# Kernel optimization log

Measured on AMD Instinct MI355X. Metric: run time of the kernel, lower is better.

## Reference

```python
import jax, jax.numpy as jnp
import numpy as np

N = 50000      # nodes
E = 400000     # edges
G = 128        # graphs in batch
D_NODE = 64
EDGE_DIM = 72
HEADS = 4
H0, H1, H2 = 128, 128, 64
NC = 2
NEG = 0.2      # GATConv leaky_relu negative_slope default
D1 = H2 + EDGE_DIM - 1  # ffn input dim = 135


def _p(k, shape, s=0.1):
    return jax.random.normal(k, shape, dtype=jnp.float32) * s


def setup_inputs() -> dict:
    key = jax.random.key(0)
    ks = jax.random.split(key, 24)
    x = jax.random.normal(ks[0], (N, D_NODE), dtype=jnp.float32)
    edge_index = jax.random.randint(ks[1], (2, E), 0, N)
    edge_attr = jax.random.uniform(ks[2], (E, EDGE_DIM), dtype=jnp.float32)
    batch = jnp.sort(jax.random.randint(ks[3], (N,), 0, G))
    return dict(
        x=x, edge_index=edge_index, edge_attr=edge_attr, batch=batch,
        # GATConv layer 1: in=D_NODE, out=H0, heads=HEADS, concat
        W1=_p(ks[4], (D_NODE, HEADS * H0)), We1=_p(ks[5], (EDGE_DIM, HEADS * H0)),
        as1=_p(ks[6], (HEADS, H0)), ad1=_p(ks[7], (HEADS, H0)), ae1=_p(ks[8], (HEADS, H0)),
        b1=jnp.zeros((HEADS * H0,), jnp.float32),
        # GATConv layer 2: in=HEADS*H0, out=H1, heads=HEADS, concat
        W2=_p(ks[9], (HEADS * H0, HEADS * H1)), We2=_p(ks[10], (EDGE_DIM, HEADS * H1)),
        as2=_p(ks[11], (HEADS, H1)), ad2=_p(ks[12], (HEADS, H1)), ae2=_p(ks[13], (HEADS, H1)),
        b2=jnp.zeros((HEADS * H1,), jnp.float32),
        # GATConv layer 3: in=HEADS*H1, out=H2, heads=1, concat=False
        W3=_p(ks[14], (HEADS * H1, H2)), We3=_p(ks[15], (EDGE_DIM, H2)),
        as3=_p(ks[16], (1, H2)), ad3=_p(ks[17], (1, H2)), ae3=_p(ks[18], (1, H2)),
        b3=jnp.zeros((H2,), jnp.float32),
        # ffn: Linear(135 -> 67), ReLU, Linear(67 -> 2), Softmax
        Wf1=_p(ks[19], (D1, D1 // 2)), bf1=jnp.zeros((D1 // 2,), jnp.float32),
        Wf2=_p(ks[20], (D1 // 2, NC)), bf2=jnp.zeros((NC,), jnp.float32),
    )


def _seg_softmax(s, seg, n):
    # numerically-stable softmax over segments (per-destination neighborhoods)
    m = jax.ops.segment_max(s, seg, num_segments=n)
    m = jnp.where(jnp.isfinite(m), m, 0.0)
    e = jnp.exp(s - m[seg])
    z = jax.ops.segment_sum(e, seg, num_segments=n)
    return e / (z[seg] + 1e-16)


def _gat(x, src, dst, eattr, W, We, a_s, a_d, a_e, b, heads, oc, concat):
    # PyG GATConv with edge_dim: shared src/dst projection, edge feats only in attention
    n = x.shape[0]
    xs = (x @ W).reshape(n, heads, oc)            # [N,H,C]
    ee = (eattr @ We).reshape(-1, heads, oc)      # [Ea,H,C]
    alpha = (xs * a_s).sum(-1)[src] + (xs * a_d).sum(-1)[dst] + (ee * a_e).sum(-1)
    alpha = jax.nn.leaky_relu(alpha, NEG)         # [Ea,H]
    alpha = _seg_softmax(alpha, dst, n)
    out = jax.ops.segment_sum(xs[src] * alpha[:, :, None], dst, num_segments=n)
    out = out.reshape(n, heads * oc) if concat else out.mean(axis=1)
    return out + b


def reference(x, edge_index, edge_attr, batch,
              W1, We1, as1, ad1, ae1, b1,
              W2, We2, as2, ad2, ae2, b2,
              W3, We3, as3, ad3, ae3, b3,
              Wf1, bf1, Wf2, bf2):
    src, dst = edge_index[0], edge_index[1]
    n = x.shape[0]
    # --- 1-gram feature vector: scatter-add edge_attr[:, :-1] by graph of src ---
    eb = batch[src]
    og = jax.ops.segment_sum(edge_attr[:, :-1], eb, num_segments=G)   # [G, EDGE_DIM-1]
    og = og / jnp.maximum(jnp.linalg.norm(og, axis=1, keepdims=True), 1e-12)
    # --- add self loops, edge_attr fill_value='mean' (mean over incoming edges) ---
    ones_e = jnp.ones((src.shape[0],), x.dtype)
    deg = jax.ops.segment_sum(ones_e, dst, num_segments=n)
    loop_attr = jax.ops.segment_sum(edge_attr, dst, num_segments=n) / jnp.maximum(deg, 1.0)[:, None]
    nodes = jnp.arange(n)
    src_a = jnp.concatenate([src, nodes])
    dst_a = jnp.concatenate([dst, nodes])
    ea = jnp.concatenate([edge_attr, loop_attr], axis=0)
    # --- GAT stack with ReLU activations ---
    h = jax.nn.relu(_gat(x, src_a, dst_a, ea, W1, We1, as1, ad1, ae1, b1, HEADS, H0, True))
    h = jax.nn.relu(_gat(h, src_a, dst_a, ea, W2, We2, as2, ad2, ae2, b2, HEADS, H1, True))
    h = jax.nn.relu(_gat(h, src_a, dst_a, ea, W3, We3, as3, ad3, ae3, b3, 1, H2, False))
    # --- global mean pool over graphs ---
    cnt = jax.ops.segment_sum(jnp.ones((n,), x.dtype), batch, num_segments=G)
    pooled = jax.ops.segment_sum(h, batch, num_segments=G) / jnp.maximum(cnt, 1.0)[:, None]
    # --- concat + ffn (dropout p=0 in eval) + softmax ---
    z = jnp.concatenate([pooled, og], axis=1)                         # [G, 135]
    z = jax.nn.relu(z @ Wf1 + bf1)
    return jax.nn.softmax(z @ Wf2 + bf2, axis=1)
```

## Files before the change

kernel.cpp:

```cpp
#include <hip/hip_runtime.h>

#define NNODES 50000
#define NEDGES 400000
#define NEA    450000
#define NG     128
#define DEGCAP 96
#define OGW    72

typedef unsigned short u16;
typedef unsigned int   u32;
typedef __attribute__((ext_vector_type(8))) short short8v;
typedef __attribute__((ext_vector_type(4))) float f32x4;

static inline int ceil_div(int a, int b){ return (a + b - 1)/b; }

__device__ __forceinline__ u16 f2bf(float f){
  u32 u = __builtin_bit_cast(u32, f);
  u = (u + 0x7fffu + ((u >> 16) & 1u)) >> 16;
  return (u16)u;
}
__device__ __forceinline__ float bfLO(u32 q){ return __builtin_bit_cast(float, q << 16); }
__device__ __forceinline__ float bfHI(u32 q){ return __builtin_bit_cast(float, q & 0xffff0000u); }
__device__ __forceinline__ void gload_lds16(const u16* g, u16* l){
  __builtin_amdgcn_global_load_lds((const __attribute__((address_space(1))) void*)g,
                                   (__attribute__((address_space(3))) void*)l, 16, 0, 0);
}

__global__ void k_prep(const float* __restrict__ x, u16* __restrict__ xb,
                       const float* __restrict__ W1, u16* __restrict__ Wt1,
                       const float* __restrict__ W2, u16* __restrict__ Wt2,
                       const float* __restrict__ W3, u16* __restrict__ Wt3,
                       const float* __restrict__ We1, const float* __restrict__ ae1,
                       const float* __restrict__ We2, const float* __restrict__ ae2,
                       const float* __restrict__ We3, const float* __restrict__ ae3,
                       float* __restrict__ veall){
  int i = blockIdx.x*blockDim.x + threadIdx.x;
  if (i < 800000){
    float4 v = ((const float4*)x)[i];
    ((ushort4*)xb)[i] = make_ushort4(f2bf(v.x), f2bf(v.y), f2bf(v.z), f2bf(v.w));
    return;
  }
  i -= 800000;
  if (i < 32768){
    int n = i >> 6, k = i & 63;
    Wt1[i] = f2bf(W1[(size_t)k*512 + n]);
    return;
  }
  i -= 32768;
  if (i < 262144){
    int n = i >> 9, k = i & 511;
    Wt2[i] = f2bf(W2[(size_t)k*512 + n]);
    return;
  }
  i -= 262144;
  if (i < 32768){
    int n = i >> 9, k = i & 511;
    Wt3[i] = f2bf(W3[(size_t)k*64 + n]);
    return;
  }
  i -= 32768;
  if (i < 648){
    const float* We; const float* ae; int H, C, basej, li;
    if (i < 288){ We = We1; ae = ae1; H = 4; C = 128; basej = 0; li = i; }
    else if (i < 576){ We = We2; ae = ae2; H = 4; C = 128; basej = 4; li = i - 288; }
    else { We = We3; ae = ae3; H = 1; C = 64; basej = 8; li = i - 576; }
    int k = li / H, h = li - k*H;
    const float* wrow = We + (size_t)k*H*C + (size_t)h*C;
    const float* arow = ae + (size_t)h*C;
    float s = 0.f;
    for (int c = 0; c < C; ++c) s += wrow[c]*arow[c];
    veall[k*9 + basej + h] = s;
  }
}

__global__ void k_deg_gb(const int* __restrict__ src, const int* __restrict__ dst,
                         const int* __restrict__ batch,
                         int* __restrict__ deg, int* __restrict__ gb, int* __restrict__ gcnt){
  __shared__ int h[NG];
  int t = threadIdx.x;
  if (t < NG) h[t] = 0;
  __syncthreads();
  int e = blockIdx.x*blockDim.x + t;
  if (e < NEDGES){
    atomicAdd(&deg[dst[e]], 1);
    int g = batch[src[e]];
    gb[e] = g;
    atomicAdd(&h[g], 1);
  }
  __syncthreads();
  if (t < NG && h[t]) atomicAdd(&gcnt[t], h[t]);
}

__global__ __launch_bounds__(1024) void k_scans(const int* __restrict__ deg, int* __restrict__ off,
                                                const int* __restrict__ gcnt, int* __restrict__ goff,
                                                int* __restrict__ gcur){
  __shared__ int s[1024];
  int t = threadIdx.x;
  if (blockIdx.x == 0){
    const int CH = (NNODES + 1023)/1024;
    int i0 = t*CH, i1 = min(i0 + CH, NNODES);
    int loc = 0;
    for (int i = i0; i < i1; ++i) loc += deg[i] + 1;
    s[t] = loc; __syncthreads();
    for (int o = 1; o < 1024; o <<= 1){
      int v = (t >= o) ? s[t-o] : 0;
      __syncthreads();
      s[t] += v;
      __syncthreads();
    }
    int excl = s[t] - loc;
    for (int i = i0; i < i1; ++i){ off[i] = excl; excl += deg[i] + 1; }
    if (t == 1023) off[NNODES] = s[1023];
  } else {
    int v = 0;
    if (t < NG){ v = gcnt[t]; s[t] = v; }
    __syncthreads();
    for (int o = 1; o < NG; o <<= 1){
      int x = 0;
      if (t < NG && t >= o) x = s[t-o];
      __syncthreads();
      if (t < NG) s[t] += x;
      __syncthreads();
    }
    if (t < NG){ goff[t] = s[t] - v; gcur[t] = s[t] - v; }
  }
}

__global__ void k_scatter(const int* __restrict__ src, const int* __restrict__ dst,
                          const int* __restrict__ gb, const int* __restrict__ off,
                          int* __restrict__ cnt, int* __restrict__ gcur,
                          int* __restrict__ csr_src, int* __restrict__ edgepos,
                          int* __restrict__ sortedeid){
  __shared__ int lcnt[NG];
  __shared__ int lbase[NG];
  int t = threadIdx.x;
  int e = blockIdx.x*256 + t;
  if (t < NG) lcnt[t] = 0;
  __syncthreads();
  int g = -1, lr = 0;
  if (e < NEDGES){
    int d = dst[e];
    int p = off[d] + atomicAdd(&cnt[d], 1);
    csr_src[p] = src[e];
    edgepos[e] = p;
    g = gb[e];
    lr = atomicAdd(&lcnt[g], 1);
  } else {
    int n2 = e - NEDGES;
    if (n2 < NNODES){
      int p = off[n2+1] - 1;
      csr_src[p] = n2;
    }
  }
  __syncthreads();
  if (t < NG && lcnt[t]) lbase[t] = atomicAdd(&gcur[t], lcnt[t]);
  __syncthreads();
  if (g >= 0) sortedeid[lbase[g] + lr] = e;
}

__global__ __launch_bounds__(256) void k_og2(const float* __restrict__ attr,
    const int* __restrict__ goff, const int* __restrict__ gcnt,
    const int* __restrict__ sortedeid, float* __restrict__ og){
  __shared__ float red[16][OGW];
  int g = blockIdx.x >> 4, chunk = blockIdx.x & 15;
  int lane = threadIdx.x & 63, w = threadIdx.x >> 6;
  int esub = lane >> 4, l16 = lane & 15;
  int slot = w*4 + esub;
  int beg = goff[g], cnt = gcnt[g];
  int cbeg = beg + ((cnt*chunk) >> 4);
  int cend = beg + ((cnt*(chunk+1)) >> 4);
  f32x4 acc  = {0.f,0.f,0.f,0.f};
  f32x4 acch = {0.f,0.f,0.f,0.f};
  for (int i0 = cbeg; i0 < cend; i0 += 32){
    int e1 = i0 + slot, e2 = i0 + 16 + slot;
    int id1 = (e1 < cend) ? sortedeid[e1] : -1;
    int id2 = (e2 < cend) ? sortedeid[e2] : -1;
    f32x4 v1 = {0.f,0.f,0.f,0.f}, v2 = {0.f,0.f,0.f,0.f};
    f32x4 h1 = {0.f,0.f,0.f,0.f}, h2 = {0.f,0.f,0.f,0.f};
    if (id1 >= 0){
      v1 = *(const f32x4*)(attr + (size_t)id1*72 + l16*4);
      if (l16 < 2) h1 = *(const f32x4*)(attr + (size_t)id1*72 + 64 + l16*4);
    }
    if (id2 >= 0){
      v2 = *(const f32x4*)(attr + (size_t)id2*72 + l16*4);
      if (l16 < 2) h2 = *(const f32x4*)(attr + (size_t)id2*72 + 64 + l16*4);
    }
    acc += v1; acc += v2;
    if (l16 < 2){ acch += h1; acch += h2; }
  }
  #pragma unroll
  for (int j = 0; j < 4; ++j) red[slot][l16*4 + j] = acc[j];
  if (l16 < 2){
    #pragma unroll
    for (int j = 0; j < 4; ++j) red[slot][64 + l16*4 + j] = acch[j];
  }
  __syncthreads();
  int t = threadIdx.x;
  if (t < 71){
    float s = 0.f;
    #pragma unroll
    for (int q = 0; q < 16; ++q) s += red[q][t];
    atomicAdd(&og[g*OGW + t], s);
  }
}

__global__ __launch_bounds__(256) void k_se_all(const float* __restrict__ attr,
    const int* __restrict__ edgepos, const float* __restrict__ veall,
    float* __restrict__ se1, float* __restrict__ se2, float* __restrict__ se3){
  __shared__ float vel[72*9];
  for (int i = threadIdx.x; i < 72*9; i += blockDim.x) vel[i] = veall[i];
  __syncthreads();
  int e = blockIdx.x*blockDim.x + threadIdx.x;
  if (e >= NEDGES) return;
  const float4* row = (const float4*)(attr + (size_t)e*72);
  float s[9];
  #pragma unroll
  for (int j = 0; j < 9; ++j) s[j] = 0.f;
  #pragma unroll
  for (int kk = 0; kk < 18; ++kk){
    float4 a = row[kk];
    #pragma unroll
    for (int j = 0; j < 9; ++j)
      s[j] += a.x*vel[(kk*4+0)*9+j] + a.y*vel[(kk*4+1)*9+j]
            + a.z*vel[(kk*4+2)*9+j] + a.w*vel[(kk*4+3)*9+j];
  }
  int p = edgepos[e];
  *(float4*)(se1 + (size_t)p*4) = make_float4(s[0], s[1], s[2], s[3]);
  *(float4*)(se2 + (size_t)p*4) = make_float4(s[4], s[5], s[6], s[7]);
  se3[p] = s[8];
}

__global__ __launch_bounds__(256) void k_gemm128(const u16* __restrict__ A,
    const u16* __restrict__ Bt, u16* __restrict__ C, int M, int K,
    const float* __restrict__ a_s, const float* __restrict__ a_d,
    float* __restrict__ ssrc, float* __restrict__ sdst){
  __shared__ __align__(16) u16 smem[128*128];
  u16* As = smem;
  u16* Bs = smem + 128*64;
  __shared__ float s_ps[128][2];
  __shared__ float s_pd[128][2];
  const int tid = threadIdx.x;
  const int wid = tid >> 6, lane = tid & 63;
  const int l15 = lane & 15, kslot = lane >> 4;
  const int wr = wid >> 1, wc = wid & 1;
  const int h = blockIdx.x;
  const int m0 = blockIdx.y * 128, n0 = h * 128;
  const int Nn = 512;
  f32x4 acc[4][4];
  #pragma unroll
  for (int mi = 0; mi < 4; ++mi)
    #pragma unroll
    for (int ni = 0; ni < 4; ++ni)
      acc[mi][ni] = (f32x4){0.f,0.f,0.f,0.f};

  for (int kt = 0; kt < K; kt += 64){
    #pragma unroll
    for (int r = 0; r < 4; ++r){
      int chunk = (r*4 + wid)*64 + lane;
      int row = chunk >> 3, c8 = chunk & 7;
      int srcc = c8 ^ (row & 7);
      int grow = m0 + row; if (grow > M-1) grow = M-1;
      gload_lds16(A + (size_t)grow*K + kt + srcc*8, &As[chunk*8]);
    }
    #pragma unroll
    for (int r = 0; r < 4; ++r){
      int chunk = (r*4 + wid)*64 + lane;
      int row = chunk >> 3, c8 = chunk & 7;
      int srcc = c8 ^ (row & 7);
      gload_lds16(Bt + (size_t)(n0+row)*K + kt + srcc*8, &Bs[chunk*8]);
    }
    __syncthreads();
    #pragma unroll
    for (int s = 0; s < 2; ++s){
      short8v a[4], b[4];
      #pragma unroll
      for (int mi = 0; mi < 4; ++mi){
        int row = wr*64 + mi*16 + l15;
        a[mi] = *(const short8v*)(&As[row*64 + (((s*4 + kslot) ^ (row&7))*8)]);
      }
      #pragma unroll
      for (int ni = 0; ni < 4; ++ni){
        int col = wc*64 + ni*16 + l15;
        b[ni] = *(const short8v*)(&Bs[col*64 + (((s*4 + kslot) ^ (col&7))*8)]);
      }
      #pragma unroll
      for (int mi = 0; mi < 4; ++mi)
        #pragma unroll
        for (int ni = 0; ni < 4; ++ni)
          acc[mi][ni] = __builtin_amdgcn_mfma_f32_16x16x32_bf16(a[mi], b[ni], acc[mi][ni], 0, 0, 0);
    }
    __syncthreads();
  }
  float asv[4], adv[4];
  #pragma unroll
  for (int ni = 0; ni < 4; ++ni){
    int c = wc*64 + ni*16 + l15;
    asv[ni] = a_s[h*128 + c];
    adv[ni] = a_d[h*128 + c];
  }
  #pragma unroll
  for (int mi = 0; mi < 4; ++mi){
    #pragma unroll
    for (int r = 0; r < 4; ++r){
      int row_l = wr*64 + mi*16 + kslot*4 + r;
      float ps = 0.f, pd = 0.f;
      #pragma unroll
      for (int ni = 0; ni < 4; ++ni){
        float v = acc[mi][ni][r];
        smem[row_l*128 + wc*64 + ni*16 + l15] = f2bf(v);
        ps += v*asv[ni];
        pd += v*adv[ni];
      }
      #pragma unroll
      for (int m = 8; m >= 1; m >>= 1){ ps += __shfl_xor(ps,m); pd += __shfl_xor(pd,m); }
      if (l15 == 0){ s_ps[row_l][wc] = ps; s_pd[row_l][wc] = pd; }
    }
  }
  __syncthreads();
  #pragma unroll
  for (int i = 0; i < 8; ++i){
    int c = i*256 + tid;
    int row = c >> 4, c16 = c & 15;
    int grow = m0 + row;
    if (grow < M)
      *(uint4*)(C + (size_t)grow*Nn + n0 + c16*8) = *(const uint4*)(&smem[row*128 + c16*8]);
  }
  if (tid < 128){
    int grow = m0 + tid;
    if (grow < M){
      ssrc[grow*4 + h] = s_ps[tid][0] + s_ps[tid][1];
      sdst[grow*4 + h] = s_pd[tid][0] + s_pd[tid][1];
    }
  }
}

__global__ __launch_bounds__(256) void k_gemm64(const u16* __restrict__ A,
    const u16* __restrict__ Bt, u16* __restrict__ C, int M,
    const float* __restrict__ a_s, const float* __restrict__ a_d,
    float* __restrict__ ssrc, float* __restrict__ sdst){
  __shared__ __align__(16) u16 As[64*64];
  __shared__ __align__(16) u16 Bs[64*64];
  const int tid = threadIdx.x;
  const int wid = tid >> 6, lane = tid & 63;
  const int l15 = lane & 15, kslot = lane >> 4;
  const int m0 = blockIdx.x * 64;
  f32x4 acc[4];
  #pragma unroll
  for (int ni = 0; ni < 4; ++ni) acc[ni] = (f32x4){0.f,0.f,0.f,0.f};
  for (int kt = 0; kt < 512; kt += 64){
    #pragma unroll
    for (int r = 0; r < 2; ++r){
      int chunk = r*256 + tid;
      int row = chunk >> 3, c8 = chunk & 7;
      int srcc = c8 ^ (row & 7);
      int grow = m0 + row; if (grow > M-1) grow = M-1;
      gload_lds16(A + (size_t)grow*512 + kt + srcc*8, &As[chunk*8]);
    }
    #pragma unroll
    for (int r = 0; r < 2; ++r){
      int chunk = r*256 + tid;
      int row = chunk >> 3, c8 = chunk & 7;
      int srcc = c8 ^ (row & 7);
      gload_lds16(Bt + (size_t)row*512 + kt + srcc*8, &Bs[chunk*8]);
    }
    __syncthreads();
    #pragma unroll
    for (int s = 0; s < 2; ++s){
      int row = wid*16 + l15;
      short8v a = *(const short8v*)(&As[row*64 + (((s*4 + kslot) ^ (row&7))*8)]);
      #pragma unroll
      for (int ni = 0; ni < 4; ++ni){
        int col = ni*16 + l15;
        short8v b = *(const short8v*)(&Bs[col*64 + (((s*4 + kslot) ^ (col&7))*8)]);
        acc[ni] = __builtin_amdgcn_mfma_f32_16x16x32_bf16(a, b, acc[ni], 0, 0, 0);
      }
    }
    __syncthreads();
  }
  #pragma unroll
  for (int r = 0; r < 4; ++r){
    int row_l = wid*16 + kslot*4 + r;
    int grow = m0 + row_l;
    float ps = 0.f, pd = 0.f;
    #pragma unroll
    for (int ni = 0; ni < 4; ++ni){
      float v = acc[ni][r];
      int c = ni*16 + l15;
      As[row_l*64 + c] = f2bf(v);
      ps += v*a_s[c];
      pd += v*a_d[c];
    }
    #pragma unroll
    for (int m = 8; m >= 1; m >>= 1){ ps += __shfl_xor(ps,m); pd += __shfl_xor(pd,m); }
    if (l15 == 0 && grow < M){ ssrc[grow] = ps; sdst[grow] = pd; }
  }
  __syncthreads();
  #pragma unroll
  for (int i = 0; i < 2; ++i){
    int c = i*256 + tid;
    int row = c >> 3, c8 = c & 7;
    int grow = m0 + row;
    if (grow < M)
      *(uint4*)(C + (size_t)grow*64 + c8*8) = *(const uint4*)(&As[row*64 + c8*8]);
  }
}

__global__ __launch_bounds__(256) void k_agg12(const u16* __restrict__ xs,
    const int* __restrict__ off, const int* __restrict__ csr_src,
    const float* __restrict__ ssrc, const float* __restrict__ sdst,
    const float* __restrict__ sep,
    const float* __restrict__ bias, u16* __restrict__ out){
  __shared__ float s_al[4][DEGCAP][4];
  __shared__ int   s_col[4][DEGCAP];
  int w = threadIdx.x >> 6, lane = threadIdx.x & 63;
  int n = blockIdx.x*4 + w;
  int beg = off[n];
  int deg = off[n+1] - beg;
  if (deg > DEGCAP) deg = DEGCAP;
  int es = lane >> 2, h = lane & 3;
  float sd = sdst[n*4+h];
  float sesum = 0.f;
  for (int e0 = 0; e0 < deg-1; e0 += 16){
    int e = e0 + es;
    if (e < deg-1){
      int col = csr_src[beg+e];
      float sr = sep[(size_t)(beg+e)*4 + h];
      sesum += sr;
      float s = ssrc[col*4+h] + sd + sr;
      s = (s > 0.f) ? s : 0.2f*s;
      s_al[w][e][h] = s;
      if (h == 0) s_col[w][e] = col;
    }
  }
  #pragma unroll
  for (int msk = 4; msk < 64; msk <<= 1) sesum += __shfl_xor(sesum, msk);
  if (es == 0){
    float slp = sesum / fmaxf((float)(deg-1), 1.0f);
    float s = ssrc[n*4+h] + sd + slp;
    s = (s > 0.f) ? s : 0.2f*s;
    s_al[w][deg-1][h] = s;
    if (h == 0) s_col[w][deg-1] = n;
  }
  float m = -1e30f;
  for (int e = es; e < deg; e += 16) m = fmaxf(m, s_al[w][e][h]);
  #pragma unroll
  for (int msk = 4; msk < 64; msk <<= 1) m = fmaxf(m, __shfl_xor(m, msk));
  float z = 0.f;
  for (int e = es; e < deg; e += 16){ float ex = __expf(s_al[w][e][h]-m); s_al[w][e][h] = ex; z += ex; }
  #pragma unroll
  for (int msk = 4; msk < 64; msk <<= 1) z += __shfl_xor(z, msk);
  float inv = 1.0f/(z + 1e-16f);
  for (int e = es; e < deg; e += 16) s_al[w][e][h] *= inv;
  int degR = (deg + 3) & ~3;
  for (int e = deg + es; e < degR; e += 16){ s_al[w][e][h] = 0.f; if (h == 0) s_col[w][e] = n; }
  __syncthreads();
  int hh = lane >> 4;
  f32x4 accA = {0.f,0.f,0.f,0.f}, accB = {0.f,0.f,0.f,0.f};
  for (int e = 0; e < degR; e += 4){
    int c0 = s_col[w][e+0], c1 = s_col[w][e+1], c2 = s_col[w][e+2], c3 = s_col[w][e+3];
    uint4 q0 = *(const uint4*)(xs + (size_t)c0*512 + lane*8);
    uint4 q1 = *(const uint4*)(xs + (size_t)c1*512 + lane*8);
    uint4 q2 = *(const uint4*)(xs + (size_t)c2*512 + lane*8);
    uint4 q3 = *(const uint4*)(xs + (size_t)c3*512 + lane*8);
    float a0 = s_al[w][e+0][hh], a1 = s_al[w][e+1][hh];
    float a2 = s_al[w][e+2][hh], a3 = s_al[w][e+3][hh];
    accA[0] += a0*bfLO(q0.x) + a1*bfLO(q1.x) + a2*bfLO(q2.x) + a3*bfLO(q3.x);
    accA[1] += a0*bfHI(q0.x) + a1*bfHI(q1.x) + a2*bfHI(q2.x) + a3*bfHI(q3.x);
    accA[2] += a0*bfLO(q0.y) + a1*bfLO(q1.y) + a2*bfLO(q2.y) + a3*bfLO(q3.y);
    accA[3] += a0*bfHI(q0.y) + a1*bfHI(q1.y) + a2*bfHI(q2.y) + a3*bfHI(q3.y);
    accB[0] += a0*bfLO(q0.z) + a1*bfLO(q1.z) + a2*bfLO(q2.z) + a3*bfLO(q3.z);
    accB[1] += a0*bfHI(q0.z) + a1*bfHI(q1.z) + a2*bfHI(q2.z) + a3*bfHI(q3.z);
    accB[2] += a0*bfLO(q0.w) + a1*bfLO(q1.w) + a2*bfLO(q2.w) + a3*bfLO(q3.w);
    accB[3] += a0*bfHI(q0.w) + a1*bfHI(q1.w) + a2*bfHI(q2.w) + a3*bfHI(q3.w);
  }
  f32x4 b0 = *(const f32x4*)(bias + lane*8);
  f32x4 b1 = *(const f32x4*)(bias + lane*8 + 4);
  short8v res;
  res[0] = (short)f2bf(fmaxf(accA[0]+b0[0], 0.f));
  res[1] = (short)f2bf(fmaxf(accA[1]+b0[1], 0.f));
  res[2] = (short)f2bf(fmaxf(accA[2]+b0[2], 0.f));
  res[3] = (short)f2bf(fmaxf(accA[3]+b0[3], 0.f));
  res[4] = (short)f2bf(fmaxf(accB[0]+b1[0], 0.f));
  res[5] = (short)f2bf(fmaxf(accB[1]+b1[1], 0.f));
  res[6] = (short)f2bf(fmaxf(accB[2]+b1[2], 0.f));
  res[7] = (short)f2bf(fmaxf(accB[3]+b1[3], 0.f));
  *(short8v*)(out + (size_t)n*512 + lane*8) = res;
}

__global__ __launch_bounds__(256) void k_agg3(const u16* __restrict__ xs,
    const int* __restrict__ off, const int* __restrict__ csr_src,
    const float* __restrict__ ssrc, const float* __restrict__ sdst,
    const float* __restrict__ se3,
    const float* __restrict__ bias, float* __restrict__ out){
  __shared__ float s_al[4][DEGCAP];
  __shared__ int   s_col[4][DEGCAP];
  int w = threadIdx.x >> 6, lane = threadIdx.x & 63;
  int n = blockIdx.x*4 + w;
  int beg = off[n];
  int deg = off[n+1] - beg;
  if (deg > DEGCAP) deg = DEGCAP;
  float sd = sdst[n];
  float sesum = 0.f;
  for (int e0 = 0; e0 < deg-1; e0 += 64){
    int e = e0 + lane;
    if (e < deg-1){
      int col = csr_src[beg+e];
      float sr = se3[beg+e];
      sesum += sr;
      float s = ssrc[col] + sd + sr;
      s = (s > 0.f) ? s : 0.2f*s;
      s_al[w][e] = s;
      s_col[w][e] = col;
    }
  }
  #pragma unroll
  for (int msk = 1; msk < 64; msk <<= 1) sesum += __shfl_xor(sesum, msk);
  if (lane == 0){
    float slp = sesum / fmaxf((float)(deg-1), 1.0f);
    float s = ssrc[n] + sd + slp;
    s = (s > 0.f) ? s : 0.2f*s;
    s_al[w][deg-1] = s;
    s_col[w][deg-1] = n;
  }
  float m = -1e30f;
  for (int e = lane; e < deg; e += 64) m = fmaxf(m, s_al[w][e]);
  #pragma unroll
  for (int msk = 1; msk < 64; msk <<= 1) m = fmaxf(m, __shfl_xor(m, msk));
  float z = 0.f;
  for (int e = lane; e < deg; e += 64){ float ex = __expf(s_al[w][e]-m); s_al[w][e] = ex; z += ex; }
  #pragma unroll
  for (int msk = 1; msk < 64; msk <<= 1) z += __shfl_xor(z, msk);
  float inv = 1.0f/(z + 1e-16f);
  for (int e = lane; e < deg; e += 64) s_al[w][e] *= inv;
  int degR = (deg + 3) & ~3;
  for (int e = deg + lane; e < degR; e += 64){ s_al[w][e] = 0.f; s_col[w][e] = n; }
  __syncthreads();
  int half = lane >> 5, cp = lane & 31;
  float a0 = 0.f, a1 = 0.f;
  for (int e = 0; e < degR; e += 4){
    int c0 = s_col[w][e + half], c1 = s_col[w][e + 2 + half];
    u32 q0 = *(const u32*)(xs + (size_t)c0*64 + cp*2);
    u32 q1 = *(const u32*)(xs + (size_t)c1*64 + cp*2);
    float al0 = s_al[w][e + half], al1 = s_al[w][e + 2 + half];
    a0 += al0*bfLO(q0) + al1*bfLO(q1);
    a1 += al0*bfHI(q0) + al1*bfHI(q1);
  }
  a0 += __shfl_xor(a0, 32);
  a1 += __shfl_xor(a1, 32);
  if (half == 0){
    float2 o;
    o.x = fmaxf(a0 + bias[cp*2+0], 0.f);
    o.y = fmaxf(a1 + bias[cp*2+1], 0.f);
    *(float2*)(out + (size_t)n*64 + cp*2) = o;
  }
}

__global__ __launch_bounds__(64) void k_pool(const float* __restrict__ h, const int* __restrict__ batch,
                                             float* __restrict__ pooled, int* __restrict__ cntg){
  int l = threadIdx.x;
  int start = blockIdx.x * 128;
  if (start >= NNODES) return;
  int endn = min(start + 128, NNODES);
  float acc = 0.f;
  int curg = batch[start];
  int run = 0;
  for (int n = start; n < endn; ++n){
    int g = batch[n];
    if (g != curg){
      atomicAdd(&pooled[curg*64+l], acc);
      if (l == 0) atomicAdd(&cntg[curg], run);
      acc = 0.f; run = 0; curg = g;
    }
    acc += h[(size_t)n*64 + l];
    ++run;
  }
  atomicAdd(&pooled[curg*64+l], acc);
  if (l == 0) atomicAdd(&cntg[curg], run);
}

__global__ void k_ffn(const float* __restrict__ pooled, const int* __restrict__ cntg,
                      const float* __restrict__ og,
                      const float* __restrict__ Wf1, const float* __restrict__ bf1,
                      const float* __restrict__ Wf2, const float* __restrict__ bf2,
                      float* __restrict__ out){
  __shared__ float z[135];
  __shared__ float z1[67];
  __shared__ float o2[2];
  int g = blockIdx.x, t = threadIdx.x;
  if (t < 64) z[t] = pooled[g*64+t] * (1.0f/fmaxf((float)cntg[g], 1.0f));
  else if (t < 135) z[t] = og[g*OGW + (t-64)];
  __syncthreads();
  if (t == 0){
    float s = 0.f;
    for (int k = 0; k < 71; ++k) s += z[64+k]*z[64+k];
    float scale = 1.0f / fmaxf(sqrtf(s), 1e-12f);
    for (int k = 0; k < 71; ++k) z[64+k] *= scale;
  }
  __syncthreads();
  if (t < 67){
    float s = bf1[t];
    for (int d = 0; d < 135; ++d) s += z[d]*Wf1[d*67+t];
    z1[t] = fmaxf(s, 0.f);
  }
  __syncthreads();
  if (t < 2){
    float s = bf2[t];
    for (int j = 0; j < 67; ++j) s += z1[j]*Wf2[j*2+t];
    o2[t] = s;
  }
  __syncthreads();
  if (t == 0){
    float m = fmaxf(o2[0], o2[1]);
    float e0 = expf(o2[0]-m), e1 = expf(o2[1]-m);
    float inv = 1.0f/(e0+e1);
    out[g*2+0] = e0*inv;
    out[g*2+1] = e1*inv;
  }
}

extern "C" void kernel_launch(void* const* d_in, const int* in_sizes, int n_in,
                              void* d_out, int out_size, void* d_ws, size_t ws_size,
                              hipStream_t stream){
  const float* x     = (const float*)d_in[0];
  const int*   ei    = (const int*)d_in[1];
  const float* eattr = (const float*)d_in[2];
  const int*   batch = (const int*)d_in[3];
  const float* W1  = (const float*)d_in[4];
  const float* We1 = (const float*)d_in[5];
  const float* as1 = (const float*)d_in[6];
  const float* ad1 = (const float*)d_in[7];
  const float* ae1 = (const float*)d_in[8];
  const float* b1  = (const float*)d_in[9];
  const float* W2  = (const float*)d_in[10];
  const float* We2 = (const float*)d_in[11];
  const float* as2 = (const float*)d_in[12];
  const float* ad2 = (const float*)d_in[13];
  const float* ae2 = (const float*)d_in[14];
  const float* b2  = (const float*)d_in[15];
  const float* W3  = (const float*)d_in[16];
  const float* We3 = (const float*)d_in[17];
  const float* as3 = (const float*)d_in[18];
  const float* ad3 = (const float*)d_in[19];
  const float* ae3 = (const float*)d_in[20];
  const float* b3  = (const float*)d_in[21];
  const float* Wf1 = (const float*)d_in[22];
  const float* bf1 = (const float*)d_in[23];
  const float* Wf2 = (const float*)d_in[24];
  const float* bf2 = (const float*)d_in[25];
  (void)in_sizes; (void)n_in; (void)out_size; (void)ws_size;
  const int* src = ei;
  const int* dst = ei + NEDGES;
  float* out = (float*)d_out;

  char* base = (char*)d_ws;
  size_t woff = 0;
  auto alloc = [&](size_t bytes)->char*{
    char* p = base + woff;
    woff += (bytes + 255) & ~(size_t)255;
    return p;
  };
  u16*   xsb    = (u16*)  alloc((size_t)NNODES*512*2);
  u16*   hb     = (u16*)  alloc((size_t)NNODES*512*2);
  u16*   xs3b   = (u16*)  alloc((size_t)NNODES*64*2);
  float* h3     = (float*)alloc((size_t)NNODES*64*4);
  u16*   xb     = (u16*)  alloc((size_t)NNODES*64*2);
  u16*   Wt1    = (u16*)  alloc((size_t)512*64*2);
  u16*   Wt2    = (u16*)  alloc((size_t)512*512*2);
  u16*   Wt3    = (u16*)  alloc((size_t)64*512*2);
  float* se1    = (float*)alloc((size_t)NEA*4*4);
  float* se2    = (float*)alloc((size_t)NEA*4*4);
  float* se3    = (float*)alloc((size_t)NEA*4);
  float* ssrc   = (float*)alloc((size_t)NNODES*4*4);
  float* sdst   = (float*)alloc((size_t)NNODES*4*4);
  float* veall  = (float*)alloc(72*9*4);
  int*   gb     = (int*)alloc((size_t)NEDGES*4);
  int*   csroff = (int*)alloc((size_t)(NNODES+1)*4);
  int*   csrsrc = (int*)alloc((size_t)NEA*4);
  int*   edgepos= (int*)alloc((size_t)NEDGES*4);
  int*   goff   = (int*)alloc(NG*4);
  int*   gcur   = (int*)alloc(NG*4);
  int*   sortedeid = (int*)alloc((size_t)NEDGES*4);
  size_t z0 = woff;
  int*   deg    = (int*)alloc((size_t)NNODES*4);
  int*   cnt    = (int*)alloc((size_t)NNODES*4);
  int*   gcnt   = (int*)alloc(NG*4);
  float* og     = (float*)alloc((size_t)NG*OGW*4);
  float* pooled = (float*)alloc((size_t)NG*64*4);
  int*   cntg   = (int*)alloc((size_t)NG*4);
  size_t zlen = woff - z0;

  hipMemsetAsync(base + z0, 0, zlen, stream);

  k_prep<<<ceil_div(800000+32768+262144+32768+648,256),256,0,stream>>>(
      x, xb, W1, Wt1, W2, Wt2, W3, Wt3, We1, ae1, We2, ae2, We3, ae3, veall);

  k_deg_gb <<<ceil_div(NEDGES,256),256,0,stream>>>(src, dst, batch, deg, gb, gcnt);
  k_scans  <<<2,1024,0,stream>>>(deg, csroff, gcnt, goff, gcur);
  k_scatter<<<ceil_div(NEDGES+NNODES,256),256,0,stream>>>(src, dst, gb, csroff, cnt, gcur,
                                                          csrsrc, edgepos, sortedeid);

  k_og2   <<<NG*16,256,0,stream>>>(eattr, goff, gcnt, sortedeid, og);
  k_se_all<<<ceil_div(NEDGES,256),256,0,stream>>>(eattr, edgepos, veall, se1, se2, se3);

  dim3 g128(4, ceil_div(NNODES,128));

  k_gemm128<<<g128,256,0,stream>>>(xb, Wt1, xsb, NNODES, 64, as1, ad1, ssrc, sdst);
  k_agg12<<<NNODES/4,256,0,stream>>>(xsb, csroff, csrsrc, ssrc, sdst, se1, b1, hb);

  k_gemm128<<<g128,256,0,stream>>>(hb, Wt2, xsb, NNODES, 512, as2, ad2, ssrc, sdst);
  k_agg12<<<NNODES/4,256,0,stream>>>(xsb, csroff, csrsrc, ssrc, sdst, se2, b2, hb);

  k_gemm64<<<ceil_div(NNODES,64),256,0,stream>>>(hb, Wt3, xs3b, NNODES, as3, ad3, ssrc, sdst);
  k_agg3<<<NNODES/4,256,0,stream>>>(xs3b, csroff, csrsrc, ssrc, sdst, se3, b3, h3);

  k_pool<<<ceil_div(NNODES,128),64,0,stream>>>(h3, batch, pooled, cntg);
  k_ffn <<<NG,192,0,stream>>>(pooled, cntg, og, Wf1, bf1, Wf2, bf2, out);
}
```

Baseline: 600.8 us.

## Parallelize CSR offset scan and merge small preprocessing kernels

```diff
diff --git a/kernel.cpp b/kernel.cpp
--- a/kernel.cpp
+++ b/kernel.cpp
@@ -6,6 +6,11 @@
 #define NG     128
 #define DEGCAP 96
 #define OGW    72
+#define NCH    49
+#define PREPN  1128328
+#define PREPB  4408
+#define EDGEB  1563
+#define OGB    (NG*16)
 
 typedef unsigned short u16;
 typedef unsigned int   u32;
@@ -26,14 +31,33 @@
                                    (__attribute__((address_space(3))) void*)l, 16, 0, 0);
 }
 
-__global__ void k_prep(const float* __restrict__ x, u16* __restrict__ xb,
+__global__ void k_prep_deg(const float* __restrict__ x, u16* __restrict__ xb,
                        const float* __restrict__ W1, u16* __restrict__ Wt1,
                        const float* __restrict__ W2, u16* __restrict__ Wt2,
                        const float* __restrict__ W3, u16* __restrict__ Wt3,
                        const float* __restrict__ We1, const float* __restrict__ ae1,
                        const float* __restrict__ We2, const float* __restrict__ ae2,
                        const float* __restrict__ We3, const float* __restrict__ ae3,
-                       float* __restrict__ veall){
+                       float* __restrict__ veall,
+                       const int* __restrict__ src, const int* __restrict__ dst,
+                       const int* __restrict__ batch,
+                       int* __restrict__ deg, int* __restrict__ gb, int* __restrict__ gcnt){
+  if (blockIdx.x >= PREPB){
+    __shared__ int h[NG];
+    int t = threadIdx.x;
+    if (t < NG) h[t] = 0;
+    __syncthreads();
+    int e = (blockIdx.x - PREPB)*256 + t;
+    if (e < NEDGES){
+      atomicAdd(&deg[dst[e]], 1);
+      int g = batch[src[e]];
+      gb[e] = g;
+      atomicAdd(&h[g], 1);
+    }
+    __syncthreads();
+    if (t < NG && h[t]) atomicAdd(&gcnt[t], h[t]);
+    return;
+  }
   int i = blockIdx.x*blockDim.x + threadIdx.x;
   if (i < 800000){
     float4 v = ((const float4*)x)[i];
@@ -73,56 +97,65 @@
   }
 }
 
-__global__ void k_deg_gb(const int* __restrict__ src, const int* __restrict__ dst,
-                         const int* __restrict__ batch,
-                         int* __restrict__ deg, int* __restrict__ gb, int* __restrict__ gcnt){
-  __shared__ int h[NG];
-  int t = threadIdx.x;
-  if (t < NG) h[t] = 0;
-  __syncthreads();
-  int e = blockIdx.x*blockDim.x + t;
-  if (e < NEDGES){
-    atomicAdd(&deg[dst[e]], 1);
-    int g = batch[src[e]];
-    gb[e] = g;
-    atomicAdd(&h[g], 1);
-  }
-  __syncthreads();
-  if (t < NG && h[t]) atomicAdd(&gcnt[t], h[t]);
-}
-
-__global__ __launch_bounds__(1024) void k_scans(const int* __restrict__ deg, int* __restrict__ off,
-                                                const int* __restrict__ gcnt, int* __restrict__ goff,
-                                                int* __restrict__ gcur){
+__global__ __launch_bounds__(1024) void k_chunksum(const int* __restrict__ deg, int* __restrict__ csum){
   __shared__ int s[1024];
   int t = threadIdx.x;
-  if (blockIdx.x == 0){
-    const int CH = (NNODES + 1023)/1024;
-    int i0 = t*CH, i1 = min(i0 + CH, NNODES);
-    int loc = 0;
-    for (int i = i0; i < i1; ++i) loc += deg[i] + 1;
-    s[t] = loc; __syncthreads();
-    for (int o = 1; o < 1024; o <<= 1){
-      int v = (t >= o) ? s[t-o] : 0;
-      __syncthreads();
-      s[t] += v;
-      __syncthreads();
-    }
-    int excl = s[t] - loc;
-    for (int i = i0; i < i1; ++i){ off[i] = excl; excl += deg[i] + 1; }
-    if (t == 1023) off[NNODES] = s[1023];
-  } else {
-    int v = 0;
-    if (t < NG){ v = gcnt[t]; s[t] = v; }
-    __syncthreads();
-    for (int o = 1; o < NG; o <<= 1){
-      int x = 0;
-      if (t < NG && t >= o) x = s[t-o];
-      __syncthreads();
-      if (t < NG) s[t] += x;
-      __syncthreads();
-    }
-    if (t < NG){ goff[t] = s[t] - v; gcur[t] = s[t] - v; }
+  int i = blockIdx.x*1024 + t;
+  s[t] = (i < NNODES) ? deg[i]+1 : 0;
+  __syncthreads();
+  for (int o = 512; o > 0; o >>= 1){
+    if (t < o) s[t] += s[t+o];
+    __syncthreads();
+  }
+  if (t == 0) csum[blockIdx.x] = s[0];
+}
+
+__global__ __launch_bounds__(128) void k_scanmid(const int* __restrict__ csum, int* __restrict__ cbase,
+                                                 const int* __restrict__ gcnt, int* __restrict__ goff,
+                                                 int* __restrict__ gcur){
+  __shared__ int sg[NG];
+  int t = threadIdx.x;
+  if (t < 64){
+    int v0 = (t < NCH) ? csum[t] : 0;
+    int v = v0;
+    #pragma unroll
+    for (int o = 1; o < 64; o <<= 1){
+      int xsh = __shfl_up(v, o);
+      if (t >= o) v += xsh;
+    }
+    if (t < NCH) cbase[t] = v - v0;
+  }
+  int vg = gcnt[t];
+  sg[t] = vg;
+  __syncthreads();
+  for (int o = 1; o < NG; o <<= 1){
+    int xg = (t >= o) ? sg[t-o] : 0;
+    __syncthreads();
+    sg[t] += xg;
+    __syncthreads();
+  }
+  goff[t] = sg[t] - vg;
+  gcur[t] = sg[t] - vg;
+}
+
+__global__ __launch_bounds__(1024) void k_scanout(const int* __restrict__ deg,
+                                                  const int* __restrict__ cbase, int* __restrict__ off){
+  __shared__ int s[1024];
+  int t = threadIdx.x;
+  int i = blockIdx.x*1024 + t;
+  int v = (i < NNODES) ? deg[i]+1 : 0;
+  s[t] = v;
+  __syncthreads();
+  for (int o = 1; o < 1024; o <<= 1){
+    int xv = (t >= o) ? s[t-o] : 0;
+    __syncthreads();
+    s[t] += xv;
+    __syncthreads();
+  }
+  if (i < NNODES){
+    int incl = s[t] + cbase[blockIdx.x];
+    off[i] = incl - v;
+    if (i == NNODES-1) off[NNODES] = incl;
   }
 }
 
@@ -158,59 +191,60 @@
   if (g >= 0) sortedeid[lbase[g] + lr] = e;
 }
 
-__global__ __launch_bounds__(256) void k_og2(const float* __restrict__ attr,
+__global__ __launch_bounds__(256) void k_edge(const float* __restrict__ attr,
     const int* __restrict__ goff, const int* __restrict__ gcnt,
-    const int* __restrict__ sortedeid, float* __restrict__ og){
-  __shared__ float red[16][OGW];
-  int g = blockIdx.x >> 4, chunk = blockIdx.x & 15;
-  int lane = threadIdx.x & 63, w = threadIdx.x >> 6;
-  int esub = lane >> 4, l16 = lane & 15;
-  int slot = w*4 + esub;
-  int beg = goff[g], cnt = gcnt[g];
-  int cbeg = beg + ((cnt*chunk) >> 4);
-  int cend = beg + ((cnt*(chunk+1)) >> 4);
-  f32x4 acc  = {0.f,0.f,0.f,0.f};
-  f32x4 acch = {0.f,0.f,0.f,0.f};
-  for (int i0 = cbeg; i0 < cend; i0 += 32){
-    int e1 = i0 + slot, e2 = i0 + 16 + slot;
-    int id1 = (e1 < cend) ? sortedeid[e1] : -1;
-    int id2 = (e2 < cend) ? sortedeid[e2] : -1;
-    f32x4 v1 = {0.f,0.f,0.f,0.f}, v2 = {0.f,0.f,0.f,0.f};
-    f32x4 h1 = {0.f,0.f,0.f,0.f}, h2 = {0.f,0.f,0.f,0.f};
-    if (id1 >= 0){
-      v1 = *(const f32x4*)(attr + (size_t)id1*72 + l16*4);
-      if (l16 < 2) h1 = *(const f32x4*)(attr + (size_t)id1*72 + 64 + l16*4);
-    }
-    if (id2 >= 0){
-      v2 = *(const f32x4*)(attr + (size_t)id2*72 + l16*4);
-      if (l16 < 2) h2 = *(const f32x4*)(attr + (size_t)id2*72 + 64 + l16*4);
-    }
-    acc += v1; acc += v2;
-    if (l16 < 2){ acch += h1; acch += h2; }
-  }
-  #pragma unroll
-  for (int j = 0; j < 4; ++j) red[slot][l16*4 + j] = acc[j];
-  if (l16 < 2){
-    #pragma unroll
-    for (int j = 0; j < 4; ++j) red[slot][64 + l16*4 + j] = acch[j];
-  }
-  __syncthreads();
-  int t = threadIdx.x;
-  if (t < 71){
-    float s = 0.f;
-    #pragma unroll
-    for (int q = 0; q < 16; ++q) s += red[q][t];
-    atomicAdd(&og[g*OGW + t], s);
-  }
-}
-
-__global__ __launch_bounds__(256) void k_se_all(const float* __restrict__ attr,
+    const int* __restrict__ sortedeid, float* __restrict__ og,
     const int* __restrict__ edgepos, const float* __restrict__ veall,
     float* __restrict__ se1, float* __restrict__ se2, float* __restrict__ se3){
-  __shared__ float vel[72*9];
+  __shared__ float sh[16*OGW];
+  if (blockIdx.x < OGB){
+    float (*red)[OGW] = (float(*)[OGW])sh;
+    int g = blockIdx.x >> 4, chunk = blockIdx.x & 15;
+    int lane = threadIdx.x & 63, w = threadIdx.x >> 6;
+    int esub = lane >> 4, l16 = lane & 15;
+    int slot = w*4 + esub;
+    int beg = goff[g], cnt = gcnt[g];
+    int cbeg = beg + ((cnt*chunk) >> 4);
+    int cend = beg + ((cnt*(chunk+1)) >> 4);
+    f32x4 acc  = {0.f,0.f,0.f,0.f};
+    f32x4 acch = {0.f,0.f,0.f,0.f};
+    for (int i0 = cbeg; i0 < cend; i0 += 32){
+      int e1 = i0 + slot, e2 = i0 + 16 + slot;
+      int id1 = (e1 < cend) ? sortedeid[e1] : -1;
+      int id2 = (e2 < cend) ? sortedeid[e2] : -1;
+      f32x4 v1 = {0.f,0.f,0.f,0.f}, v2 = {0.f,0.f,0.f,0.f};
+      f32x4 h1 = {0.f,0.f,0.f,0.f}, h2 = {0.f,0.f,0.f,0.f};
+      if (id1 >= 0){
+        v1 = *(const f32x4*)(attr + (size_t)id1*72 + l16*4);
+        if (l16 < 2) h1 = *(const f32x4*)(attr + (size_t)id1*72 + 64 + l16*4);
+      }
+      if (id2 >= 0){
+        v2 = *(const f32x4*)(attr + (size_t)id2*72 + l16*4);
+        if (l16 < 2) h2 = *(const f32x4*)(attr + (size_t)id2*72 + 64 + l16*4);
+      }
+      acc += v1; acc += v2;
+      if (l16 < 2){ acch += h1; acch += h2; }
+    }
+    #pragma unroll
+    for (int j = 0; j < 4; ++j) red[slot][l16*4 + j] = acc[j];
+    if (l16 < 2){
+      #pragma unroll
+      for (int j = 0; j < 4; ++j) red[slot][64 + l16*4 + j] = acch[j];
+    }
+    __syncthreads();
+    int t = threadIdx.x;
+    if (t < 71){
+      float s = 0.f;
+      #pragma unroll
+      for (int q = 0; q < 16; ++q) s += red[q][t];
+      atomicAdd(&og[g*OGW + t], s);
+    }
+    return;
+  }
+  float* vel = sh;
   for (int i = threadIdx.x; i < 72*9; i += blockDim.x) vel[i] = veall[i];
   __syncthreads();
-  int e = blockIdx.x*blockDim.x + threadIdx.x;
+  int e = (blockIdx.x - OGB)*blockDim.x + threadIdx.x;
   if (e >= NEDGES) return;
   const float4* row = (const float4*)(attr + (size_t)e*72);
   float s[9];
@@ -680,6 +714,8 @@
   int*   goff   = (int*)alloc(NG*4);
   int*   gcur   = (int*)alloc(NG*4);
   int*   sortedeid = (int*)alloc((size_t)NEDGES*4);
+  int*   csum   = (int*)alloc(NCH*4);
+  int*   cbase  = (int*)alloc(NCH*4);
   size_t z0 = woff;
   int*   deg    = (int*)alloc((size_t)NNODES*4);
   int*   cnt    = (int*)alloc((size_t)NNODES*4);
@@ -691,16 +727,19 @@
 
   hipMemsetAsync(base + z0, 0, zlen, stream);
 
-  k_prep<<<ceil_div(800000+32768+262144+32768+648,256),256,0,stream>>>(
-      x, xb, W1, Wt1, W2, Wt2, W3, Wt3, We1, ae1, We2, ae2, We3, ae3, veall);
-
-  k_deg_gb <<<ceil_div(NEDGES,256),256,0,stream>>>(src, dst, batch, deg, gb, gcnt);
-  k_scans  <<<2,1024,0,stream>>>(deg, csroff, gcnt, goff, gcur);
+  k_prep_deg<<<PREPB + EDGEB,256,0,stream>>>(
+      x, xb, W1, Wt1, W2, Wt2, W3, Wt3, We1, ae1, We2, ae2, We3, ae3, veall,
+      src, dst, batch, deg, gb, gcnt);
+
+  k_chunksum<<<NCH,1024,0,stream>>>(deg, csum);
+  k_scanmid <<<1,128,0,stream>>>(csum, cbase, gcnt, goff, gcur);
+  k_scanout <<<NCH,1024,0,stream>>>(deg, cbase, csroff);
+
   k_scatter<<<ceil_div(NEDGES+NNODES,256),256,0,stream>>>(src, dst, gb, csroff, cnt, gcur,
                                                           csrsrc, edgepos, sortedeid);
 
-  k_og2   <<<NG*16,256,0,stream>>>(eattr, goff, gcnt, sortedeid, og);
-  k_se_all<<<ceil_div(NEDGES,256),256,0,stream>>>(eattr, edgepos, veall, se1, se2, se3);
+  k_edge<<<OGB + EDGEB,256,0,stream>>>(eattr, goff, gcnt, sortedeid, og,
+                                       edgepos, veall, se1, se2, se3);
 
   dim3 g128(4, ceil_div(NNODES,128));
 
```

After: 515.2 us. 1.17x faster.
